# Kernel tuning notes

Hardware: AMD Instinct MI355X
Metric: run time of the kernel (lower is better)

## Reference

```python
import jax, jax.numpy as jnp
import numpy as np

BN_EPS = 1e-3  # Keras BatchNormalization default epsilon


def setup_inputs() -> dict:
    key = jax.random.key(0)
    ks = jax.random.split(key, 8)
    N, F, H, S, E = 30000, 16, 16, 8, 300000
    return {
        "x": jax.random.normal(ks[0], (N, F), dtype=jnp.float32),
        "e": jax.random.uniform(ks[1], (E, S), dtype=jnp.float32),
        "src": jax.random.randint(ks[2], (E,), 0, N),
        "dst": jax.random.randint(ks[3], (E,), 0, N),
        "Wk": jax.random.normal(ks[4], (S, F * H), dtype=jnp.float32) * 0.1,
        "bk": jnp.zeros((F * H,), dtype=jnp.float32),
        "Wr": jax.random.normal(ks[5], (F, H), dtype=jnp.float32) * 0.1,
        "br": jnp.zeros((H,), dtype=jnp.float32),
        "gamma": jnp.ones((H,), dtype=jnp.float32),
        "beta": jnp.zeros((H,), dtype=jnp.float32),
        "mmean": jnp.zeros((H,), dtype=jnp.float32),
        "mvar": jnp.ones((H,), dtype=jnp.float32),
        "Wd": jax.random.normal(ks[6], (H, 3), dtype=jnp.float32) * 0.1,
        "bd": jnp.zeros((3,), dtype=jnp.float32),
    }


def reference(x, e, src, dst, Wk, bk, Wr, br, gamma, beta, mmean, mvar, Wd, bd):
    N, F = x.shape
    H = Wr.shape[1]
    # ECCConv: per-edge filter generated from edge features -> [E, F, H]
    kernels = (e @ Wk + bk).reshape(e.shape[0], F, H)
    # message: gather source node feats, apply per-edge kernel
    msg = jnp.einsum('ef,efh->eh', x[src], kernels)  # [E, H]
    # scatter-sum aggregate to target nodes
    agg = jax.ops.segment_sum(msg, dst, num_segments=N)  # [N, H]
    h = jax.nn.relu(agg + x @ Wr + br)
    # BatchNormalization (inference: moving stats); Dropout = identity at eval
    h = (h - mmean) / jnp.sqrt(mvar + BN_EPS) * gamma + beta
    pooled = jnp.max(h, axis=0, keepdims=True)  # GlobalMaxPool, single mode -> [1, H]
    return pooled @ Wd + bd  # [1, 3]
```

## Files before the change

### kernel.cpp

```cpp
#include <hip/hip_runtime.h>

#define BN_EPS 1e-3f

typedef float vf4 __attribute__((ext_vector_type(4)));
typedef _Float16 half8 __attribute__((ext_vector_type(8)));

__device__ __forceinline__ unsigned int f2k(float f) {
    unsigned int u = __float_as_uint(f);
    return (u & 0x80000000u) ? ~u : (u | 0x80000000u);
}
__device__ __forceinline__ float k2f(unsigned int u) {
    return __uint_as_float((u & 0x80000000u) ? (u & 0x7FFFFFFFu) : ~u);
}

template <int S, int F, int H>
__global__ void node_pre(const float* __restrict__ x,
                         const float* __restrict__ Wk,
                         const float* __restrict__ bk,
                         const float* __restrict__ Wr,
                         const float* __restrict__ br,
                         _Float16* __restrict__ y2h,
                         float* __restrict__ agg,
                         unsigned int* __restrict__ pooled_u,
                         int N) {
    if (blockIdx.x == 0 && threadIdx.x < H) pooled_u[threadIdx.x] = 0u;

    int t = blockIdx.x * blockDim.x + threadIdx.x;
    int n = t / H;
    int h = t % H;
    if (n >= N) return;

    float xf[F];
#pragma unroll
    for (int f = 0; f < F; ++f) xf[f] = x[n * F + f];

    _Float16* yrow = y2h + (size_t)n * (S + 1) * H + h;
#pragma unroll
    for (int s = 0; s < S; ++s) {
        float acc = 0.f;
#pragma unroll
        for (int f = 0; f < F; ++f) acc += xf[f] * Wk[(s * F + f) * H + h];
        yrow[s * H] = (_Float16)acc;
    }

    float accb = 0.f, accr = 0.f;
#pragma unroll
    for (int f = 0; f < F; ++f) {
        accb += xf[f] * bk[f * H + h];
        accr += xf[f] * Wr[f * H + h];
    }
    yrow[S * H] = (_Float16)accb;
    agg[(size_t)n * H + h] = accr + br[h];
}

template <int S, int H>
__global__ void __launch_bounds__(256)
edge_scatter(const float* __restrict__ efeat,
             const int* __restrict__ src,
             const int* __restrict__ dst,
             const _Float16* __restrict__ y2h,
             float* __restrict__ agg,
             int E) {
    constexpr int EB = 256;
    constexpr int LDW = EB + 4;
    __shared__ float msg[H][LDW];
    __shared__ int sdst[EB];

    int t = threadIdx.x;
    int e0 = blockIdx.x * EB;

    int el = t >> 1;
    int hi = t & 1;
    int ell0 = el, ell1 = el + 128;
    int ec0 = min(e0 + ell0, E - 1);
    int ec1 = min(e0 + ell1, E - 1);

    int sn0 = __builtin_nontemporal_load(src + ec0);
    int sn1 = __builtin_nontemporal_load(src + ec1);
    if (hi == 0) {
        sdst[ell0] = __builtin_nontemporal_load(dst + ec0);
        sdst[ell1] = __builtin_nontemporal_load(dst + ec1);
    }

    const vf4* e40 = (const vf4*)(efeat + (size_t)ec0 * S);
    const vf4* e41 = (const vf4*)(efeat + (size_t)ec1 * S);
    vf4 ea0 = __builtin_nontemporal_load(e40);
    vf4 eb0 = __builtin_nontemporal_load(e40 + 1);
    vf4 ea1 = __builtin_nontemporal_load(e41);
    vf4 eb1 = __builtin_nontemporal_load(e41 + 1);
    float es0[S + 1] = {ea0.x, ea0.y, ea0.z, ea0.w, eb0.x, eb0.y, eb0.z, eb0.w, 1.0f};
    float es1[S + 1] = {ea1.x, ea1.y, ea1.z, ea1.w, eb1.x, eb1.y, eb1.z, eb1.w, 1.0f};

    const _Float16* yb0 = y2h + (size_t)sn0 * (S + 1) * H + hi * 8;
    const _Float16* yb1 = y2h + (size_t)sn1 * (S + 1) * H + hi * 8;

    float m0[8] = {0.f, 0.f, 0.f, 0.f, 0.f, 0.f, 0.f, 0.f};
    float m1[8] = {0.f, 0.f, 0.f, 0.f, 0.f, 0.f, 0.f, 0.f};
#pragma unroll
    for (int s = 0; s <= S; ++s) {
        half8 hv0 = *(const half8*)(yb0 + s * H);
        half8 hv1 = *(const half8*)(yb1 + s * H);
#pragma unroll
        for (int j = 0; j < 8; ++j) {
            m0[j] += es0[s] * (float)hv0[j];
            m1[j] += es1[s] * (float)hv1[j];
        }
    }
#pragma unroll
    for (int j = 0; j < 8; ++j) {
        msg[hi * 8 + j][ell0] = m0[j];
        msg[hi * 8 + j][ell1] = m1[j];
    }

    __syncthreads();

    int e2 = t >> 4;
    int h = t & 15;
#pragma unroll
    for (int p = 0; p < 16; ++p) {
        int el2 = p * 16 + e2;
        if (e0 + el2 < E) {
            unsafeAtomicAdd(&agg[(size_t)sdst[el2] * H + h], msg[h][el2]);
        }
    }
}

template <int H>
__global__ void __launch_bounds__(256)
bn_relu_max(const float* __restrict__ agg,
            const float* __restrict__ gamma,
            const float* __restrict__ beta,
            const float* __restrict__ mmean,
            const float* __restrict__ mvar,
            unsigned int* __restrict__ pooled_u,
            int N) {
    __shared__ unsigned int smax[H];
    if (threadIdx.x < H) smax[threadIdx.x] = 0u;
    __syncthreads();

    int t = blockIdx.x * blockDim.x + threadIdx.x;
    int stride = gridDim.x * blockDim.x;
    int h4 = (t & 3) * 4;

    float sc[4], sh[4];
#pragma unroll
    for (int j = 0; j < 4; ++j) {
        float s = gamma[h4 + j] * rsqrtf(mvar[h4 + j] + BN_EPS);
        sc[j] = s;
        sh[j] = beta[h4 + j] - mmean[h4 + j] * s;
    }

    float best[4] = {-INFINITY, -INFINITY, -INFINITY, -INFINITY};
    int total4 = N * H / 4;
    const vf4* agg4 = (const vf4*)agg;
    for (int i = t; i < total4; i += stride) {
        vf4 v = agg4[i];
#pragma unroll
        for (int j = 0; j < 4; ++j) {
            float w = v[j] > 0.f ? v[j] : 0.f;
            w = w * sc[j] + sh[j];
            best[j] = fmaxf(best[j], w);
        }
    }
#pragma unroll
    for (int j = 0; j < 4; ++j) atomicMax(&smax[h4 + j], f2k(best[j]));
    __syncthreads();
    if (threadIdx.x < H) atomicMax(&pooled_u[threadIdx.x], smax[threadIdx.x]);
}

template <int H>
__global__ void final_matvec(const unsigned int* __restrict__ pooled_u,
                             const float* __restrict__ Wd,
                             const float* __restrict__ bd,
                             float* __restrict__ out,
                             int HOUT) {
    int j = threadIdx.x;
    if (j >= HOUT) return;
    float acc = bd[j];
#pragma unroll
    for (int hh = 0; hh < H; ++hh) acc += k2f(pooled_u[hh]) * Wd[hh * HOUT + j];
    out[j] = acc;
}

extern "C" void kernel_launch(void* const* d_in, const int* in_sizes, int n_in,
                              void* d_out, int out_size, void* d_ws, size_t ws_size,
                              hipStream_t stream) {
    const float* x     = (const float*)d_in[0];
    const float* e     = (const float*)d_in[1];
    const int*   src   = (const int*)d_in[2];
    const int*   dst   = (const int*)d_in[3];
    const float* Wk    = (const float*)d_in[4];
    const float* bk    = (const float*)d_in[5];
    const float* Wr    = (const float*)d_in[6];
    const float* br    = (const float*)d_in[7];
    const float* gamma = (const float*)d_in[8];
    const float* beta  = (const float*)d_in[9];
    const float* mmean = (const float*)d_in[10];
    const float* mvar  = (const float*)d_in[11];
    const float* Wd    = (const float*)d_in[12];
    const float* bd    = (const float*)d_in[13];

    constexpr int S = 8, F = 16, H = 16;
    const int E = in_sizes[2];
    const int N = in_sizes[0] / F;
    const int HOUT = in_sizes[13];

    _Float16* y2h = (_Float16*)d_ws;
    float* agg = (float*)(y2h + (size_t)N * (S + 1) * H);
    unsigned int* pooled_u = (unsigned int*)(agg + (size_t)N * H);

    const int T = 256;
    int nh = N * H;
    node_pre<S, F, H><<<(nh + T - 1) / T, T, 0, stream>>>(
        x, Wk, bk, Wr, br, y2h, agg, pooled_u, N);

    int eblocks = (E + 255) / 256;
    edge_scatter<S, H><<<eblocks, T, 0, stream>>>(
        e, src, dst, y2h, agg, E);

    bn_relu_max<H><<<1024, T, 0, stream>>>(agg, gamma, beta, mmean, mvar, pooled_u, N);

    final_matvec<H><<<1, 64, 0, stream>>>(pooled_u, Wd, bd, (float*)d_out, HOUT);
}
```

Before: 142.1 us.

## Replace node precompute with per-edge MFMA message kernel and fused base/BN pass

Drops the per-node fp16 precompute of x·Wk. Each wave now takes a tile of 16 edges and forms the messages directly with 16x16x32 f16 MFMA, where A is e_s·x[src] (plus x for the bias term) and B is Wk/bk held in registers. The residual x·Wr+br is moved into the BN/ReLU/max kernel, and agg is zeroed with a memset. This removes one kernel and its intermediate buffer, but the edge kernel now issues atomics straight from MFMA accumulators without an LDS transpose and rounds the activation products to fp16.

```diff
diff --git a/kernel.cpp b/kernel.cpp
--- a/kernel.cpp
+++ b/kernel.cpp
@@ -3,7 +3,8 @@
 #define BN_EPS 1e-3f
 
 typedef float vf4 __attribute__((ext_vector_type(4)));
-typedef _Float16 half8 __attribute__((ext_vector_type(8)));
+typedef float f32x4 __attribute__((ext_vector_type(4)));
+typedef _Float16 half8v __attribute__((ext_vector_type(8)));
 
 __device__ __forceinline__ unsigned int f2k(float f) {
     unsigned int u = __float_as_uint(f);
@@ -14,151 +15,110 @@
 }
 
 template <int S, int F, int H>
-__global__ void node_pre(const float* __restrict__ x,
-                         const float* __restrict__ Wk,
-                         const float* __restrict__ bk,
-                         const float* __restrict__ Wr,
-                         const float* __restrict__ br,
-                         _Float16* __restrict__ y2h,
-                         float* __restrict__ agg,
-                         unsigned int* __restrict__ pooled_u,
-                         int N) {
-    if (blockIdx.x == 0 && threadIdx.x < H) pooled_u[threadIdx.x] = 0u;
+__global__ void __launch_bounds__(256)
+edge_mfma(const float* __restrict__ efeat,
+          const int* __restrict__ src,
+          const int* __restrict__ dst,
+          const float* __restrict__ x,
+          const float* __restrict__ Wk,
+          const float* __restrict__ bk,
+          float* __restrict__ agg,
+          int E) {
+    const int lane = threadIdx.x & 63;
+    const int g = lane >> 4;
+    const int er = lane & 15;
 
-    int t = blockIdx.x * blockDim.x + threadIdx.x;
-    int n = t / H;
-    int h = t % H;
-    if (n >= N) return;
-
-    float xf[F];
+    half8v bfr[5];
 #pragma unroll
-    for (int f = 0; f < F; ++f) xf[f] = x[n * F + f];
-
-    _Float16* yrow = y2h + (size_t)n * (S + 1) * H + h;
+    for (int fr = 0; fr < 5; ++fr) {
 #pragma unroll
-    for (int s = 0; s < S; ++s) {
-        float acc = 0.f;
-#pragma unroll
-        for (int f = 0; f < F; ++f) acc += xf[f] * Wk[(s * F + f) * H + h];
-        yrow[s * H] = (_Float16)acc;
+        for (int j = 0; j < 8; ++j) {
+            int k = fr * 32 + g * 8 + j;
+            float w = 0.f;
+            if (k < S * F) w = Wk[k * H + er];
+            else if (k < S * F + F) w = bk[(k - S * F) * H + er];
+            bfr[fr][j] = (_Float16)w;
+        }
     }
 
-    float accb = 0.f, accr = 0.f;
+    const int TILES = (E + 15) >> 4;
+    int wid = blockIdx.x * (blockDim.x >> 6) + (threadIdx.x >> 6);
+    int wstride = gridDim.x * (blockDim.x >> 6);
+
+    for (int t = wid; t < TILES; t += wstride) {
+        int e0 = t << 4;
+        int eA = min(e0 + er, E - 1);
+        int sn = __builtin_nontemporal_load(src + eA);
+
+        const vf4* xp = (const vf4*)(x + (size_t)sn * F + (g & 1) * 8);
+        vf4 xa = xp[0], xb = xp[1];
+        float xh[8] = {xa.x, xa.y, xa.z, xa.w, xb.x, xb.y, xb.z, xb.w};
+
+        f32x4 acc = {0.f, 0.f, 0.f, 0.f};
 #pragma unroll
-    for (int f = 0; f < F; ++f) {
-        accb += xf[f] * bk[f * H + h];
-        accr += xf[f] * Wr[f * H + h];
-    }
-    yrow[S * H] = (_Float16)accb;
-    agg[(size_t)n * H + h] = accr + br[h];
-}
+        for (int fr = 0; fr < 4; ++fr) {
+            float es = __builtin_nontemporal_load(
+                efeat + (size_t)eA * S + fr * 2 + (g >> 1));
+            half8v a;
+#pragma unroll
+            for (int j = 0; j < 8; ++j) a[j] = (_Float16)(es * xh[j]);
+            acc = __builtin_amdgcn_mfma_f32_16x16x32_f16(a, bfr[fr], acc, 0, 0, 0);
+        }
+        {
+            half8v a;
+#pragma unroll
+            for (int j = 0; j < 8; ++j)
+                a[j] = (g < 2) ? (_Float16)xh[j] : (_Float16)0.f;
+            acc = __builtin_amdgcn_mfma_f32_16x16x32_f16(a, bfr[4], acc, 0, 0, 0);
+        }
 
-template <int S, int H>
-__global__ void __launch_bounds__(256)
-edge_scatter(const float* __restrict__ efeat,
-             const int* __restrict__ src,
-             const int* __restrict__ dst,
-             const _Float16* __restrict__ y2h,
-             float* __restrict__ agg,
-             int E) {
-    constexpr int EB = 256;
-    constexpr int LDW = EB + 4;
-    __shared__ float msg[H][LDW];
-    __shared__ int sdst[EB];
-
-    int t = threadIdx.x;
-    int e0 = blockIdx.x * EB;
-
-    int el = t >> 1;
-    int hi = t & 1;
-    int ell0 = el, ell1 = el + 128;
-    int ec0 = min(e0 + ell0, E - 1);
-    int ec1 = min(e0 + ell1, E - 1);
-
-    int sn0 = __builtin_nontemporal_load(src + ec0);
-    int sn1 = __builtin_nontemporal_load(src + ec1);
-    if (hi == 0) {
-        sdst[ell0] = __builtin_nontemporal_load(dst + ec0);
-        sdst[ell1] = __builtin_nontemporal_load(dst + ec1);
-    }
-
-    const vf4* e40 = (const vf4*)(efeat + (size_t)ec0 * S);
-    const vf4* e41 = (const vf4*)(efeat + (size_t)ec1 * S);
-    vf4 ea0 = __builtin_nontemporal_load(e40);
-    vf4 eb0 = __builtin_nontemporal_load(e40 + 1);
-    vf4 ea1 = __builtin_nontemporal_load(e41);
-    vf4 eb1 = __builtin_nontemporal_load(e41 + 1);
-    float es0[S + 1] = {ea0.x, ea0.y, ea0.z, ea0.w, eb0.x, eb0.y, eb0.z, eb0.w, 1.0f};
-    float es1[S + 1] = {ea1.x, ea1.y, ea1.z, ea1.w, eb1.x, eb1.y, eb1.z, eb1.w, 1.0f};
-
-    const _Float16* yb0 = y2h + (size_t)sn0 * (S + 1) * H + hi * 8;
-    const _Float16* yb1 = y2h + (size_t)sn1 * (S + 1) * H + hi * 8;
-
-    float m0[8] = {0.f, 0.f, 0.f, 0.f, 0.f, 0.f, 0.f, 0.f};
-    float m1[8] = {0.f, 0.f, 0.f, 0.f, 0.f, 0.f, 0.f, 0.f};
 #pragma unroll
-    for (int s = 0; s <= S; ++s) {
-        half8 hv0 = *(const half8*)(yb0 + s * H);
-        half8 hv1 = *(const half8*)(yb1 + s * H);
-#pragma unroll
-        for (int j = 0; j < 8; ++j) {
-            m0[j] += es0[s] * (float)hv0[j];
-            m1[j] += es1[s] * (float)hv1[j];
-        }
-    }
-#pragma unroll
-    for (int j = 0; j < 8; ++j) {
-        msg[hi * 8 + j][ell0] = m0[j];
-        msg[hi * 8 + j][ell1] = m1[j];
-    }
-
-    __syncthreads();
-
-    int e2 = t >> 4;
-    int h = t & 15;
-#pragma unroll
-    for (int p = 0; p < 16; ++p) {
-        int el2 = p * 16 + e2;
-        if (e0 + el2 < E) {
-            unsafeAtomicAdd(&agg[(size_t)sdst[el2] * H + h], msg[h][el2]);
+        for (int r = 0; r < 4; ++r) {
+            int ei = e0 + g * 4 + r;
+            if (ei < E) {
+                int dn = dst[ei];
+                unsafeAtomicAdd(&agg[(size_t)dn * H + er], acc[r]);
+            }
         }
     }
 }
 
-template <int H>
+template <int F, int H>
 __global__ void __launch_bounds__(256)
-bn_relu_max(const float* __restrict__ agg,
-            const float* __restrict__ gamma,
-            const float* __restrict__ beta,
-            const float* __restrict__ mmean,
-            const float* __restrict__ mvar,
-            unsigned int* __restrict__ pooled_u,
-            int N) {
+base_bn_relu_max(const float* __restrict__ agg,
+                 const float* __restrict__ x,
+                 const float* __restrict__ Wr,
+                 const float* __restrict__ br,
+                 const float* __restrict__ gamma,
+                 const float* __restrict__ beta,
+                 const float* __restrict__ mmean,
+                 const float* __restrict__ mvar,
+                 unsigned int* __restrict__ pooled_u,
+                 int N) {
     __shared__ unsigned int smax[H];
     if (threadIdx.x < H) smax[threadIdx.x] = 0u;
     __syncthreads();
 
-    int t = blockIdx.x * blockDim.x + threadIdx.x;
-    int stride = gridDim.x * blockDim.x;
-    int h4 = (t & 3) * 4;
-
-    float sc[4], sh[4];
-#pragma unroll
-    for (int j = 0; j < 4; ++j) {
-        float s = gamma[h4 + j] * rsqrtf(mvar[h4 + j] + BN_EPS);
-        sc[j] = s;
-        sh[j] = beta[h4 + j] - mmean[h4 + j] * s;
-    }
-
+    int i = blockIdx.x * blockDim.x + threadIdx.x;
+    int h4 = (i & 3) * 4;
     float best[4] = {-INFINITY, -INFINITY, -INFINITY, -INFINITY};
-    int total4 = N * H / 4;
-    const vf4* agg4 = (const vf4*)agg;
-    for (int i = t; i < total4; i += stride) {
-        vf4 v = agg4[i];
+    if (i < N * 4) {
+        int n = i >> 2;
+        const vf4* xr = (const vf4*)(x + (size_t)n * F);
+        vf4 x0 = xr[0], x1 = xr[1], x2 = xr[2], x3 = xr[3];
+        float xf[16] = {x0.x, x0.y, x0.z, x0.w, x1.x, x1.y, x1.z, x1.w,
+                        x2.x, x2.y, x2.z, x2.w, x3.x, x3.y, x3.z, x3.w};
+        vf4 a = ((const vf4*)agg)[i];
 #pragma unroll
         for (int j = 0; j < 4; ++j) {
-            float w = v[j] > 0.f ? v[j] : 0.f;
-            w = w * sc[j] + sh[j];
+            int h = h4 + j;
+            float base = br[h];
+#pragma unroll
+            for (int f = 0; f < F; ++f) base += xf[f] * Wr[f * H + h];
+            float w = a[j] + base;
+            w = w > 0.f ? w : 0.f;
+            float s = gamma[h] * rsqrtf(mvar[h] + BN_EPS);
+            w = w * s + (beta[h] - mmean[h] * s);
             best[j] = fmaxf(best[j], w);
         }
     }
@@ -205,20 +165,20 @@
     const int N = in_sizes[0] / F;
     const int HOUT = in_sizes[13];
 
-    _Float16* y2h = (_Float16*)d_ws;
-    float* agg = (float*)(y2h + (size_t)N * (S + 1) * H);
+    float* agg = (float*)d_ws;
     unsigned int* pooled_u = (unsigned int*)(agg + (size_t)N * H);
 
+    hipMemsetAsync(d_ws, 0, (size_t)N * H * sizeof(float) + H * sizeof(unsigned int),
+                   stream);
+
     const int T = 256;
-    int nh = N * H;
-    node_pre<S, F, H><<<(nh + T - 1) / T, T, 0, stream>>>(
-        x, Wk, bk, Wr, br, y2h, agg, pooled_u, N);
+    int TILES = (E + 15) / 16;
+    int eblocks = (TILES + 15) / 16;
+    edge_mfma<S, F, H><<<eblocks, T, 0, stream>>>(e, src, dst, x, Wk, bk, agg, E);
 
-    int eblocks = (E + 255) / 256;
-    edge_scatter<S, H><<<eblocks, T, 0, stream>>>(
-        e, src, dst, y2h, agg, E);
-
-    bn_relu_max<H><<<1024, T, 0, stream>>>(agg, gamma, beta, mmean, mvar, pooled_u, N);
+    int bblocks = (N * 4 + T - 1) / T;
+    base_bn_relu_max<F, H><<<bblocks, T, 0, stream>>>(
+        agg, x, Wr, br, gamma, beta, mmean, mvar, pooled_u, N);
 
     final_matvec<H><<<1, 64, 0, stream>>>(pooled_u, Wd, bd, (float*)d_out, HOUT);
 }
```

Result: faster. 121.7 us (-14.3%).
